# Kernel tuning notes

Hardware: AMD Instinct MI355X
Metric: run time of the kernel (lower is better)

The kernel has to match this reference:

```python
import jax, jax.numpy as jnp
import numpy as np

B, L, E, H, FF = 2, 2048, 1024, 16, 4096
DH = E // H
EPS = 1e-5
# NOTE: source has attn_scale = 1 / dh**(-0.5) == sqrt(dh) (multiplies, not divides)
ATTN_SCALE = float(DH) ** 0.5


def _layernorm(x, w, b):
    mu = jnp.mean(x, axis=-1, keepdims=True)
    var = jnp.mean((x - mu) ** 2, axis=-1, keepdims=True)
    return (x - mu) * jax.lax.rsqrt(var + EPS) * w + b


def setup_inputs() -> dict:
    key = jax.random.key(0)
    ks = jax.random.split(key, 8)
    s = 0.02
    return {
        "x": jax.random.normal(ks[0], (B, L, E), jnp.float32),
        "ln1_w": jnp.ones((E,), jnp.float32),
        "ln1_b": jnp.zeros((E,), jnp.float32),
        "wq": jax.random.normal(ks[1], (E, E), jnp.float32) * s,
        "bq": jnp.zeros((E,), jnp.float32),
        "wk": jax.random.normal(ks[2], (E, E), jnp.float32) * s,
        "bk": jnp.zeros((E,), jnp.float32),
        "wv": jax.random.normal(ks[3], (E, E), jnp.float32) * s,
        "bv": jnp.zeros((E,), jnp.float32),
        "wo": jax.random.normal(ks[4], (E, E), jnp.float32) * s,
        "bo": jnp.zeros((E,), jnp.float32),
        "ln2_w": jnp.ones((E,), jnp.float32),
        "ln2_b": jnp.zeros((E,), jnp.float32),
        "wu": jax.random.normal(ks[5], (E, FF), jnp.float32) * s,
        "bu": jnp.zeros((FF,), jnp.float32),
        "wd": jax.random.normal(ks[6], (FF, E), jnp.float32) * s,
        "bd": jnp.zeros((E,), jnp.float32),
    }


def reference(x, ln1_w, ln1_b, wq, bq, wk, bk, wv, bv, wo, bo,
              ln2_w, ln2_b, wu, bu, wd, bd):
    # --- attention block (pre-LN, manual softmax attention) ---
    xn = _layernorm(x, ln1_w, ln1_b)                       # [B,L,E]
    q = (xn @ wq + bq).reshape(B, L, H, DH)
    k = (xn @ wk + bk).reshape(B, L, H, DH)
    v = (xn @ wv + bv).reshape(B, L, H, DH)
    score = jnp.einsum("blhd,bmhd->bhlm", q, k) * ATTN_SCALE  # [B,H,L,L]
    attn = jax.nn.softmax(score, axis=-1)
    ctx = jnp.einsum("bhlm,bmhd->blhd", attn, v).reshape(B, L, E)
    hidden = x + (ctx @ wo + bo)
    # --- FFN block (pre-LN, GELU) ---
    hn = _layernorm(hidden, ln2_w, ln2_b)
    up = jax.nn.gelu(hn @ wu + bu, approximate=False)      # [B,L,F]
    down = up @ wd + bd
    return hidden + down
```

## Files before the change

kernel.cpp:

```cpp
#include <hip/hip_runtime.h>
#include <stdint.h>


typedef __attribute__((ext_vector_type(8))) short short8;
typedef __attribute__((ext_vector_type(4))) float floatx4;

#define MFMA_BF16(a, b, c) __builtin_amdgcn_mfma_f32_16x16x32_bf16((a), (b), (c), 0, 0, 0)

__device__ __forceinline__ unsigned short f2bf(float f) {
  union { float f; unsigned int u; } v; v.f = f;
  unsigned int r = v.u + 0x7FFFu + ((v.u >> 16) & 1u);
  return (unsigned short)(r >> 16);
}

__device__ __forceinline__ unsigned int f2u(float f) {
  union { float f; unsigned int u; } v; v.f = f; return v.u;
}

__device__ __forceinline__ void gl_lds16(const unsigned short* g, unsigned short* l) {
  __builtin_amdgcn_global_load_lds(
      (const __attribute__((address_space(1))) unsigned int*)g,
      (__attribute__((address_space(3))) unsigned int*)l, 16, 0, 0);
}

template <int MODE, int BN>
__global__ __launch_bounds__(256)
void gemm_bt(const unsigned short* __restrict__ A,
             const unsigned short* __restrict__ Bt,
             const float* __restrict__ bias,
             void* __restrict__ outp,
             const float* __restrict__ res,
             int K,
             void* __restrict__ out2, void* __restrict__ out3,
             const float* __restrict__ bias2, const float* __restrict__ bias3) {
  constexpr int BM = 128, BK = 32;
  constexpr int MI = (BN == 128) ? 4 : 2;
  constexpr int NI = 4;
  __shared__ __align__(16) unsigned short As[BM * BK];
  __shared__ __align__(16) unsigned short Bs[BN * BK];
  const int tid = threadIdx.x;
  const int wave = tid >> 6, lane = tid & 63, l16 = lane & 15, quad = lane >> 4;
  const int m0 = blockIdx.y * BM, n0 = blockIdx.x * BN;
  const int wm = (BN == 128) ? (wave >> 1) * 64 : wave * 32;
  const int wn = (BN == 128) ? (wave & 1) * 64 : 0;
  const int sA = (l16 >> 1) & 3;

  floatx4 acc[MI][NI] = {};

  for (int k0 = 0; k0 < K; k0 += BK) {
    __syncthreads();
#pragma unroll
    for (int c = 0; c < (BM * BK) / 2048; ++c) {
      const int e = (c * 256 + tid) * 8;
      const int row = e >> 5, c4 = (e >> 3) & 3;
      gl_lds16(A + (size_t)(m0 + row) * K + k0 + ((c4 ^ ((row >> 1) & 3)) << 3), &As[e]);
    }
#pragma unroll
    for (int c = 0; c < (BN * BK) / 2048; ++c) {
      const int e = (c * 256 + tid) * 8;
      const int row = e >> 5, c4 = (e >> 3) & 3;
      gl_lds16(Bt + (size_t)(n0 + row) * K + k0 + ((c4 ^ ((row >> 1) & 3)) << 3), &Bs[e]);
    }
    __syncthreads();

    short8 af[MI], bf[NI];
#pragma unroll
    for (int i = 0; i < MI; ++i)
      af[i] = *(const short8*)&As[(wm + i * 16 + l16) * BK + ((quad ^ sA) << 3)];
#pragma unroll
    for (int i = 0; i < NI; ++i)
      bf[i] = *(const short8*)&Bs[(wn + i * 16 + l16) * BK + ((quad ^ sA) << 3)];
#pragma unroll
    for (int mi = 0; mi < MI; ++mi)
#pragma unroll
      for (int ni = 0; ni < NI; ++ni)
        acc[mi][ni] = MFMA_BF16(af[mi], bf[ni], acc[mi][ni]);
  }

  const int seg = (MODE == 0) ? (n0 >> 10) : 0;
  const float* bptr = bias;
  if constexpr (MODE == 0) bptr = (seg == 0) ? bias : (seg == 1 ? bias2 : bias3);

  float bcol[NI];
#pragma unroll
  for (int ni = 0; ni < NI; ++ni) {
    const int n = n0 + wn + ni * 16 + l16;
    bcol[ni] = bptr[(MODE == 0) ? (n & 1023) : n];
  }

#pragma unroll
  for (int mi = 0; mi < MI; ++mi) {
#pragma unroll
    for (int r = 0; r < 4; ++r) {
      const int m = m0 + wm + mi * 16 + quad * 4 + r;
#pragma unroll
      for (int ni = 0; ni < NI; ++ni) {
        const int n = n0 + wn + ni * 16 + l16;
        const float c = acc[mi][ni][r] + bcol[ni];
        if constexpr (MODE == 0) {
          const int b_ = m >> 11, l = m & 2047, hd = n & 1023;
          const size_t idx =
              ((size_t)((b_ * 16 + (hd >> 6)) * 2048 + l)) * 64 + (hd & 63);
          if (seg == 0)       ((unsigned short*)outp)[idx] = f2bf(c * 8.0f);
          else if (seg == 1)  ((unsigned short*)out2)[idx] = f2bf(c);
          else                ((unsigned short*)out3)[idx] = f2bf(c);
        } else if constexpr (MODE == 1) {
          ((float*)outp)[(size_t)m * 1024 + n] = res[(size_t)m * 1024 + n] + c;
        } else if constexpr (MODE == 2) {
          const float g = 0.5f * c * (1.0f + erff(c * 0.70710678118654752f));
          ((unsigned short*)outp)[(size_t)m * 4096 + n] = f2bf(g);
        } else {
          ((float*)outp)[(size_t)m * 1024 + n] = res[(size_t)m * 1024 + n] + c;
        }
      }
    }
  }
}

__global__ __launch_bounds__(256)
void layernorm_kernel(const float* __restrict__ x, const float* __restrict__ w,
                      const float* __restrict__ b, unsigned short* __restrict__ out) {
  const int row = blockIdx.x, tid = threadIdx.x;
  const int wave = tid >> 6, lane = tid & 63;
  const float4 v = ((const float4*)(x + (size_t)row * 1024))[tid];
  float s = v.x + v.y + v.z + v.w;
  float s2 = v.x * v.x + v.y * v.y + v.z * v.z + v.w * v.w;
#pragma unroll
  for (int off = 32; off > 0; off >>= 1) {
    s += __shfl_down(s, off);
    s2 += __shfl_down(s2, off);
  }
  __shared__ float red[8];
  if (lane == 0) { red[wave] = s; red[4 + wave] = s2; }
  __syncthreads();
  const float ts = red[0] + red[1] + red[2] + red[3];
  const float ts2 = red[4] + red[5] + red[6] + red[7];
  const float mu = ts * (1.0f / 1024.0f);
  const float var = ts2 * (1.0f / 1024.0f) - mu * mu;
  const float rs = rsqrtf(var + 1e-5f);
  const float4 wv = ((const float4*)w)[tid];
  const float4 bv = ((const float4*)b)[tid];
  ushort4 o;
  o.x = f2bf((v.x - mu) * rs * wv.x + bv.x);
  o.y = f2bf((v.y - mu) * rs * wv.y + bv.y);
  o.z = f2bf((v.z - mu) * rs * wv.z + bv.z);
  o.w = f2bf((v.w - mu) * rs * wv.w + bv.w);
  ((ushort4*)(out + (size_t)row * 1024))[tid] = o;
}

__global__ __launch_bounds__(256)
void transpose_cast(const float* __restrict__ in, unsigned short* __restrict__ out,
                    int R, int C) {
  __shared__ float tile[32][33];
  const int tx = threadIdx.x, ty = threadIdx.y;
  const int c0 = blockIdx.x * 32, r0 = blockIdx.y * 32;
#pragma unroll
  for (int i = 0; i < 4; ++i)
    tile[ty + 8 * i][tx] = in[(size_t)(r0 + ty + 8 * i) * C + c0 + tx];
  __syncthreads();
#pragma unroll
  for (int i = 0; i < 4; ++i)
    out[(size_t)(c0 + ty + 8 * i) * R + r0 + tx] = f2bf(tile[tx][ty + 8 * i]);
}

__global__ __launch_bounds__(256)
void transpose_bf16(const unsigned short* __restrict__ in,
                    unsigned short* __restrict__ out, int R, int C) {
  __shared__ unsigned short tile[32][33];
  const size_t hoff = (size_t)blockIdx.z * R * C;
  in += hoff; out += hoff;
  const int tx = threadIdx.x, ty = threadIdx.y;
  const int c0 = blockIdx.x * 32, r0 = blockIdx.y * 32;
#pragma unroll
  for (int i = 0; i < 4; ++i)
    tile[ty + 8 * i][tx] = in[(size_t)(r0 + ty + 8 * i) * C + c0 + tx];
  __syncthreads();
#pragma unroll
  for (int i = 0; i < 4; ++i)
    out[(size_t)(c0 + ty + 8 * i) * R + r0 + tx] = tile[tx][ty + 8 * i];
}

__global__ __launch_bounds__(256)
void flash_attn(const unsigned short* __restrict__ q,
                const unsigned short* __restrict__ k,
                const unsigned short* __restrict__ v,
                unsigned short* __restrict__ ctx) {
  __shared__ __align__(16) unsigned short Ks[2][64 * 64];
  __shared__ __align__(16) unsigned short Vs[2][64 * 64];
  __shared__ __align__(16) unsigned short Ps[4][16 * 72];
  const int bh = blockIdx.y, qt = blockIdx.x;
  const int tid = threadIdx.x, wave = tid >> 6, lane = tid & 63;
  const int l16 = lane & 15, quad = lane >> 4;
  const unsigned short* kb = k + (size_t)bh * 2048 * 64;
  const unsigned short* vb = v + (size_t)bh * 64 * 2048;
  const int qrow = qt * 64 + wave * 16 + l16;
  const unsigned short* qp = q + (size_t)bh * 2048 * 64 + (size_t)qrow * 64;
  const short8 qf0 = *(const short8*)(qp + quad * 8);
  const short8 qf1 = *(const short8*)(qp + 32 + quad * 8);

  floatx4 O[4] = {};
  float m_run = -1e30f, l_run = 0.f;

  auto stage = [&](int t, int bufi) {
    const int kv0 = t * 64;
#pragma unroll
    for (int c = 0; c < 2; ++c) {
      const int e = (c * 256 + tid) * 8;
      const int r = e >> 6, ch = (e >> 3) & 7;
      const int sc = ((ch ^ (r & 7)) << 3);
      gl_lds16(kb + (size_t)(kv0 + r) * 64 + sc, &Ks[bufi][e]);
      gl_lds16(vb + (size_t)r * 2048 + kv0 + sc, &Vs[bufi][e]);
    }
  };
  stage(0, 0);

  for (int t = 0; t < 32; ++t) {
    __syncthreads();
    const int bufi = t & 1;
    if (t + 1 < 32) stage(t + 1, bufi ^ 1);

    floatx4 st[4];
#pragma unroll
    for (int nt = 0; nt < 4; ++nt) {
      const int r0 = nt * 16 + l16;
      const int sw = r0 & 7;
      const short8 kf0 = *(const short8*)&Ks[bufi][r0 * 64 + ((quad ^ sw) << 3)];
      const short8 kf1 = *(const short8*)&Ks[bufi][r0 * 64 + (((quad + 4) ^ sw) << 3)];
      floatx4 z = {};
      z = MFMA_BF16(kf0, qf0, z);
      z = MFMA_BF16(kf1, qf1, z);
      st[nt] = z;
    }

    float mx = st[0][0];
#pragma unroll
    for (int nt = 0; nt < 4; ++nt)
#pragma unroll
      for (int r = 0; r < 4; ++r) mx = fmaxf(mx, st[nt][r]);
    mx = fmaxf(mx, __shfl_xor(mx, 16));
    mx = fmaxf(mx, __shfl_xor(mx, 32));
    const float m_new = fmaxf(m_run, mx);
    const float alpha = __expf(m_run - m_new);
    m_run = m_new;

    float rsum = 0.f;
#pragma unroll
    for (int nt = 0; nt < 4; ++nt) {
      const float p0 = __expf(st[nt][0] - m_new);
      const float p1 = __expf(st[nt][1] - m_new);
      const float p2 = __expf(st[nt][2] - m_new);
      const float p3 = __expf(st[nt][3] - m_new);
      rsum += (p0 + p1) + (p2 + p3);
      uint2 pk;
      pk.x = __builtin_amdgcn_perm(f2u(p1), f2u(p0), 0x07060302u);
      pk.y = __builtin_amdgcn_perm(f2u(p3), f2u(p2), 0x07060302u);
      *(uint2*)&Ps[wave][l16 * 72 + nt * 16 + quad * 4] = pk;
    }
    rsum += __shfl_xor(rsum, 16);
    rsum += __shfl_xor(rsum, 32);
    l_run = l_run * alpha + rsum;

#pragma unroll
    for (int nt = 0; nt < 4; ++nt) {
      O[nt][0] *= alpha; O[nt][1] *= alpha; O[nt][2] *= alpha; O[nt][3] *= alpha;
    }

    const short8 pf0 = *(const short8*)&Ps[wave][l16 * 72 + quad * 8];
    const short8 pf1 = *(const short8*)&Ps[wave][l16 * 72 + 32 + quad * 8];
#pragma unroll
    for (int nt = 0; nt < 4; ++nt) {
      const int r0 = nt * 16 + l16;
      const int sw = r0 & 7;
      const short8 vf0 = *(const short8*)&Vs[bufi][r0 * 64 + ((quad ^ sw) << 3)];
      const short8 vf1 = *(const short8*)&Vs[bufi][r0 * 64 + (((quad + 4) ^ sw) << 3)];
      O[nt] = MFMA_BF16(vf0, pf0, O[nt]);
      O[nt] = MFMA_BF16(vf1, pf1, O[nt]);
    }
  }

  const float inv = 1.0f / l_run;
  const int b_ = bh >> 4, h = bh & 15;
  unsigned short* op = ctx + ((size_t)(b_ * 2048) + qrow) * 1024 + h * 64;
#pragma unroll
  for (int nt = 0; nt < 4; ++nt) {
    ushort4 o4;
    o4.x = f2bf(O[nt][0] * inv);
    o4.y = f2bf(O[nt][1] * inv);
    o4.z = f2bf(O[nt][2] * inv);
    o4.w = f2bf(O[nt][3] * inv);
    *(ushort4*)(op + nt * 16 + quad * 4) = o4;
  }
}

extern "C" void kernel_launch(void* const* d_in, const int* in_sizes, int n_in,
                              void* d_out, int out_size, void* d_ws, size_t ws_size,
                              hipStream_t stream) {
  const float* x     = (const float*)d_in[0];
  const float* ln1_w = (const float*)d_in[1];
  const float* ln1_b = (const float*)d_in[2];
  const float* wq    = (const float*)d_in[3];
  const float* bq    = (const float*)d_in[4];
  const float* wk    = (const float*)d_in[5];
  const float* bk    = (const float*)d_in[6];
  const float* wv    = (const float*)d_in[7];
  const float* bv    = (const float*)d_in[8];
  const float* wo    = (const float*)d_in[9];
  const float* bo    = (const float*)d_in[10];
  const float* ln2_w = (const float*)d_in[11];
  const float* ln2_b = (const float*)d_in[12];
  const float* wu    = (const float*)d_in[13];
  const float* bu    = (const float*)d_in[14];
  const float* wd    = (const float*)d_in[15];
  const float* bd    = (const float*)d_in[16];

  char* W = (char*)d_ws;
  const size_t MB = 1ull << 20;
  unsigned short* wqkvT = (unsigned short*)(W + 0 * MB);
  unsigned short* woT   = (unsigned short*)(W + 6 * MB);
  unsigned short* wuT   = (unsigned short*)(W + 8 * MB);
  unsigned short* wdT   = (unsigned short*)(W + 16 * MB);
  unsigned short* xn    = (unsigned short*)(W + 24 * MB);
  unsigned short* qb    = (unsigned short*)(W + 32 * MB);
  unsigned short* kb    = (unsigned short*)(W + 40 * MB);
  unsigned short* vb    = (unsigned short*)(W + 48 * MB);
  unsigned short* cx    = (unsigned short*)(W + 56 * MB);
  float*          hid   = (float*)(W + 64 * MB);
  unsigned short* up    = (unsigned short*)(W + 24 * MB);

  const dim3 tb(32, 8);
  transpose_cast<<<dim3(32, 32), tb, 0, stream>>>(wq, wqkvT, 1024, 1024);
  transpose_cast<<<dim3(32, 32), tb, 0, stream>>>(wk, wqkvT + 1024 * 1024, 1024, 1024);
  transpose_cast<<<dim3(32, 32), tb, 0, stream>>>(wv, wqkvT + 2048 * 1024, 1024, 1024);
  transpose_cast<<<dim3(32, 32), tb, 0, stream>>>(wo, woT, 1024, 1024);
  transpose_cast<<<dim3(128, 32), tb, 0, stream>>>(wu, wuT, 1024, 4096);
  transpose_cast<<<dim3(32, 128), tb, 0, stream>>>(wd, wdT, 4096, 1024);

  layernorm_kernel<<<4096, 256, 0, stream>>>(x, ln1_w, ln1_b, xn);
  gemm_bt<0, 128><<<dim3(24, 32), 256, 0, stream>>>(
      xn, wqkvT, bq, qb, nullptr, 1024, kb, cx, bk, bv);
  transpose_bf16<<<dim3(2, 64, 32), tb, 0, stream>>>(cx, vb, 2048, 64);
  flash_attn<<<dim3(32, 32), 256, 0, stream>>>(qb, kb, vb, cx);
  gemm_bt<1, 64><<<dim3(16, 32), 256, 0, stream>>>(
      cx, woT, bo, hid, x, 1024, nullptr, nullptr, nullptr, nullptr);

  layernorm_kernel<<<4096, 256, 0, stream>>>(hid, ln2_w, ln2_b, cx);
  gemm_bt<2, 128><<<dim3(32, 32), 256, 0, stream>>>(
      cx, wuT, bu, up, nullptr, 1024, nullptr, nullptr, nullptr, nullptr);
  gemm_bt<3, 64><<<dim3(16, 32), 256, 0, stream>>>(
      up, wdT, bd, d_out, hid, 4096, nullptr, nullptr, nullptr, nullptr);
}
```

Before: 450.9 us.

## Load K/V fragments directly into registers, use exp2 softmax, widen GEMM K-tile

Result: slower. 559.6 us (+24.1%).

```diff
diff --git a/kernel.cpp b/kernel.cpp
--- a/kernel.cpp
+++ b/kernel.cpp
@@ -4,6 +4,9 @@
 
 typedef __attribute__((ext_vector_type(8))) short short8;
 typedef __attribute__((ext_vector_type(4))) float floatx4;
+
+extern "C" __device__ float __ocml_native_exp2_f32(float);
+#define EXP2(x) __ocml_native_exp2_f32(x)
 
 #define MFMA_BF16(a, b, c) __builtin_amdgcn_mfma_f32_16x16x32_bf16((a), (b), (c), 0, 0, 0)
 
@@ -33,7 +36,7 @@
              int K,
              void* __restrict__ out2, void* __restrict__ out3,
              const float* __restrict__ bias2, const float* __restrict__ bias3) {
-  constexpr int BM = 128, BK = 32;
+  constexpr int BM = 128, BK = 64;
   constexpr int MI = (BN == 128) ? 4 : 2;
   constexpr int NI = 4;
   __shared__ __align__(16) unsigned short As[BM * BK];
@@ -43,7 +46,9 @@
   const int m0 = blockIdx.y * BM, n0 = blockIdx.x * BN;
   const int wm = (BN == 128) ? (wave >> 1) * 64 : wave * 32;
   const int wn = (BN == 128) ? (wave & 1) * 64 : 0;
-  const int sA = (l16 >> 1) & 3;
+  const int sw = l16 & 7;
+  const int sl0 = (quad ^ sw) << 3;
+  const int sl1 = sl0 ^ 32;
 
   floatx4 acc[MI][NI] = {};
 
@@ -52,29 +57,35 @@
 #pragma unroll
     for (int c = 0; c < (BM * BK) / 2048; ++c) {
       const int e = (c * 256 + tid) * 8;
-      const int row = e >> 5, c4 = (e >> 3) & 3;
-      gl_lds16(A + (size_t)(m0 + row) * K + k0 + ((c4 ^ ((row >> 1) & 3)) << 3), &As[e]);
+      const int row = e >> 6, c8 = (e >> 3) & 7;
+      gl_lds16(A + (size_t)(m0 + row) * K + k0 + ((c8 ^ (row & 7)) << 3), &As[e]);
     }
 #pragma unroll
     for (int c = 0; c < (BN * BK) / 2048; ++c) {
       const int e = (c * 256 + tid) * 8;
-      const int row = e >> 5, c4 = (e >> 3) & 3;
-      gl_lds16(Bt + (size_t)(n0 + row) * K + k0 + ((c4 ^ ((row >> 1) & 3)) << 3), &Bs[e]);
+      const int row = e >> 6, c8 = (e >> 3) & 7;
+      gl_lds16(Bt + (size_t)(n0 + row) * K + k0 + ((c8 ^ (row & 7)) << 3), &Bs[e]);
     }
     __syncthreads();
 
-    short8 af[MI], bf[NI];
-#pragma unroll
-    for (int i = 0; i < MI; ++i)
-      af[i] = *(const short8*)&As[(wm + i * 16 + l16) * BK + ((quad ^ sA) << 3)];
-#pragma unroll
-    for (int i = 0; i < NI; ++i)
-      bf[i] = *(const short8*)&Bs[(wn + i * 16 + l16) * BK + ((quad ^ sA) << 3)];
+    short8 af0[MI], af1[MI], bf0[NI], bf1[NI];
+#pragma unroll
+    for (int i = 0; i < MI; ++i) {
+      af0[i] = *(const short8*)&As[(wm + i * 16 + l16) * BK + sl0];
+      af1[i] = *(const short8*)&As[(wm + i * 16 + l16) * BK + sl1];
+    }
+#pragma unroll
+    for (int i = 0; i < NI; ++i) {
+      bf0[i] = *(const short8*)&Bs[(wn + i * 16 + l16) * BK + sl0];
+      bf1[i] = *(const short8*)&Bs[(wn + i * 16 + l16) * BK + sl1];
+    }
 #pragma unroll
     for (int mi = 0; mi < MI; ++mi)
 #pragma unroll
-      for (int ni = 0; ni < NI; ++ni)
-        acc[mi][ni] = MFMA_BF16(af[mi], bf[ni], acc[mi][ni]);
+      for (int ni = 0; ni < NI; ++ni) {
+        acc[mi][ni] = MFMA_BF16(af0[mi], bf0[ni], acc[mi][ni]);
+        acc[mi][ni] = MFMA_BF16(af1[mi], bf1[ni], acc[mi][ni]);
+      }
   }
 
   const int seg = (MODE == 0) ? (n0 >> 10) : 0;
@@ -101,7 +112,7 @@
           const int b_ = m >> 11, l = m & 2047, hd = n & 1023;
           const size_t idx =
               ((size_t)((b_ * 16 + (hd >> 6)) * 2048 + l)) * 64 + (hd & 63);
-          if (seg == 0)       ((unsigned short*)outp)[idx] = f2bf(c * 8.0f);
+          if (seg == 0)       ((unsigned short*)outp)[idx] = f2bf(c * 11.5415603270f);
           else if (seg == 1)  ((unsigned short*)out2)[idx] = f2bf(c);
           else                ((unsigned short*)out3)[idx] = f2bf(c);
         } else if constexpr (MODE == 1) {
@@ -180,55 +191,54 @@
     out[(size_t)(c0 + ty + 8 * i) * R + r0 + tx] = tile[tx][ty + 8 * i];
 }
 
-__global__ __launch_bounds__(256)
+__global__ __launch_bounds__(256, 3)
 void flash_attn(const unsigned short* __restrict__ q,
                 const unsigned short* __restrict__ k,
                 const unsigned short* __restrict__ v,
                 unsigned short* __restrict__ ctx) {
-  __shared__ __align__(16) unsigned short Ks[2][64 * 64];
-  __shared__ __align__(16) unsigned short Vs[2][64 * 64];
   __shared__ __align__(16) unsigned short Ps[4][16 * 72];
   const int bh = blockIdx.y, qt = blockIdx.x;
   const int tid = threadIdx.x, wave = tid >> 6, lane = tid & 63;
   const int l16 = lane & 15, quad = lane >> 4;
-  const unsigned short* kb = k + (size_t)bh * 2048 * 64;
-  const unsigned short* vb = v + (size_t)bh * 64 * 2048;
   const int qrow = qt * 64 + wave * 16 + l16;
   const unsigned short* qp = q + (size_t)bh * 2048 * 64 + (size_t)qrow * 64;
   const short8 qf0 = *(const short8*)(qp + quad * 8);
   const short8 qf1 = *(const short8*)(qp + 32 + quad * 8);
+  const unsigned short* kp = k + (size_t)bh * 2048 * 64 + (size_t)l16 * 64 + quad * 8;
+  const unsigned short* vp = v + (size_t)bh * 64 * 2048 + (size_t)l16 * 2048 + quad * 8;
 
   floatx4 O[4] = {};
   float m_run = -1e30f, l_run = 0.f;
 
-  auto stage = [&](int t, int bufi) {
+  short8 kc[8];
+#pragma unroll
+  for (int nt = 0; nt < 4; ++nt) {
+    kc[2 * nt]     = *(const short8*)(kp + (size_t)(nt * 16) * 64);
+    kc[2 * nt + 1] = *(const short8*)(kp + (size_t)(nt * 16) * 64 + 32);
+  }
+
+  for (int t = 0; t < 32; ++t) {
     const int kv0 = t * 64;
-#pragma unroll
-    for (int c = 0; c < 2; ++c) {
-      const int e = (c * 256 + tid) * 8;
-      const int r = e >> 6, ch = (e >> 3) & 7;
-      const int sc = ((ch ^ (r & 7)) << 3);
-      gl_lds16(kb + (size_t)(kv0 + r) * 64 + sc, &Ks[bufi][e]);
-      gl_lds16(vb + (size_t)r * 2048 + kv0 + sc, &Vs[bufi][e]);
-    }
-  };
-  stage(0, 0);
-
-  for (int t = 0; t < 32; ++t) {
-    __syncthreads();
-    const int bufi = t & 1;
-    if (t + 1 < 32) stage(t + 1, bufi ^ 1);
+    const int kvn = (t < 31) ? kv0 + 64 : 0;
+    short8 kn[8];
+#pragma unroll
+    for (int nt = 0; nt < 4; ++nt) {
+      kn[2 * nt]     = *(const short8*)(kp + (size_t)(kvn + nt * 16) * 64);
+      kn[2 * nt + 1] = *(const short8*)(kp + (size_t)(kvn + nt * 16) * 64 + 32);
+    }
+    short8 vf[8];
+#pragma unroll
+    for (int nt = 0; nt < 4; ++nt) {
+      vf[2 * nt]     = *(const short8*)(vp + (size_t)(nt * 16) * 2048 + kv0);
+      vf[2 * nt + 1] = *(const short8*)(vp + (size_t)(nt * 16) * 2048 + kv0 + 32);
+    }
 
     floatx4 st[4];
 #pragma unroll
     for (int nt = 0; nt < 4; ++nt) {
-      const int r0 = nt * 16 + l16;
-      const int sw = r0 & 7;
-      const short8 kf0 = *(const short8*)&Ks[bufi][r0 * 64 + ((quad ^ sw) << 3)];
-      const short8 kf1 = *(const short8*)&Ks[bufi][r0 * 64 + (((quad + 4) ^ sw) << 3)];
       floatx4 z = {};
-      z = MFMA_BF16(kf0, qf0, z);
-      z = MFMA_BF16(kf1, qf1, z);
+      z = MFMA_BF16(kc[2 * nt], qf0, z);
+      z = MFMA_BF16(kc[2 * nt + 1], qf1, z);
       st[nt] = z;
     }
 
@@ -240,16 +250,16 @@
     mx = fmaxf(mx, __shfl_xor(mx, 16));
     mx = fmaxf(mx, __shfl_xor(mx, 32));
     const float m_new = fmaxf(m_run, mx);
-    const float alpha = __expf(m_run - m_new);
+    const float alpha = EXP2(m_run - m_new);
     m_run = m_new;
 
     float rsum = 0.f;
 #pragma unroll
     for (int nt = 0; nt < 4; ++nt) {
-      const float p0 = __expf(st[nt][0] - m_new);
-      const float p1 = __expf(st[nt][1] - m_new);
-      const float p2 = __expf(st[nt][2] - m_new);
-      const float p3 = __expf(st[nt][3] - m_new);
+      const float p0 = EXP2(st[nt][0] - m_new);
+      const float p1 = EXP2(st[nt][1] - m_new);
+      const float p2 = EXP2(st[nt][2] - m_new);
+      const float p3 = EXP2(st[nt][3] - m_new);
       rsum += (p0 + p1) + (p2 + p3);
       uint2 pk;
       pk.x = __builtin_amdgcn_perm(f2u(p1), f2u(p0), 0x07060302u);
@@ -269,13 +279,11 @@
     const short8 pf1 = *(const short8*)&Ps[wave][l16 * 72 + 32 + quad * 8];
 #pragma unroll
     for (int nt = 0; nt < 4; ++nt) {
-      const int r0 = nt * 16 + l16;
-      const int sw = r0 & 7;
-      const short8 vf0 = *(const short8*)&Vs[bufi][r0 * 64 + ((quad ^ sw) << 3)];
-      const short8 vf1 = *(const short8*)&Vs[bufi][r0 * 64 + (((quad + 4) ^ sw) << 3)];
-      O[nt] = MFMA_BF16(vf0, pf0, O[nt]);
-      O[nt] = MFMA_BF16(vf1, pf1, O[nt]);
-    }
+      O[nt] = MFMA_BF16(vf[2 * nt], pf0, O[nt]);
+      O[nt] = MFMA_BF16(vf[2 * nt + 1], pf1, O[nt]);
+    }
+#pragma unroll
+    for (int i = 0; i < 8; ++i) kc[i] = kn[i];
   }
 
   const float inv = 1.0f / l_run;
```
